# Performance work log

Hardware: AMD Instinct MI355X
Metric: run time of the kernel (lower is better)

The kernel has to match this reference:

```python
import jax, jax.numpy as jnp
from jax import lax
import numpy as np

MAXMAG = 10.0   # max_residue_magnitude
DG = 16         # deformable_groups
K = 9           # 3x3 kernel taps


def _conv(x, w, b):
    return lax.conv_general_dilated(x, w, (1, 1), 'SAME',
                                    dimension_numbers=('NCHW', 'OIHW', 'NCHW')) + b[None, :, None, None]


def _lrelu(v):
    return jnp.where(v >= 0, v, 0.1 * v)


def _sample(img, py, px):
    # img [C,H,W]; py,px [K,H,W] absolute sample coords; bilinear, zeros outside (torchvision semantics)
    H, W = img.shape[1], img.shape[2]
    y0 = jnp.floor(py)
    x0 = jnp.floor(px)
    wy1 = py - y0
    wx1 = px - x0

    def gather(yi, xi):
        valid = ((yi >= 0) & (yi < H) & (xi >= 0) & (xi < W)).astype(img.dtype)
        yc = jnp.clip(yi, 0, H - 1).astype(jnp.int32)
        xc = jnp.clip(xi, 0, W - 1).astype(jnp.int32)
        return img[:, yc, xc] * valid[None]  # [C,K,H,W]

    v00 = gather(y0, x0)
    v01 = gather(y0, x0 + 1)
    v10 = gather(y0 + 1, x0)
    v11 = gather(y0 + 1, x0 + 1)
    return (v00 * ((1 - wy1) * (1 - wx1))[None] + v01 * ((1 - wy1) * wx1)[None]
            + v10 * (wy1 * (1 - wx1))[None] + v11 * (wy1 * wx1)[None])


def setup_inputs() -> dict:
    key = jax.random.key(0)
    ks = jax.random.split(key, 12)
    N, CIN, COUT, H, W = 4, 128, 64, 96, 96
    f = lambda k, sh, s: jax.random.normal(k, sh, dtype=jnp.float32) * s
    return {
        'x': f(ks[0], (N, CIN, H, W), 1.0),
        'extra_feat': f(ks[1], (N, 3 * COUT, H, W), 1.0),
        'flow_1': f(ks[2], (N, 2, H, W), 2.0),
        'flow_2': f(ks[3], (N, 2, H, W), 2.0),
        'w_off0': f(ks[4], (COUT, 3 * COUT + 4, 3, 3), 0.02), 'b_off0': jnp.zeros((COUT,), jnp.float32),
        'w_off1': f(ks[5], (COUT, COUT, 3, 3), 0.04), 'b_off1': jnp.zeros((COUT,), jnp.float32),
        'w_off2': f(ks[6], (COUT, COUT, 3, 3), 0.04), 'b_off2': jnp.zeros((COUT,), jnp.float32),
        'w_off3': f(ks[7], (27 * DG, COUT, 3, 3), 0.02), 'b_off3': jnp.zeros((27 * DG,), jnp.float32),
        'w_dcn': f(ks[8], (COUT, CIN, 3, 3), 0.03), 'b_dcn': jnp.zeros((COUT,), jnp.float32),
    }


def reference(x, extra_feat, flow_1, flow_2, w_off0, b_off0, w_off1, b_off1,
              w_off2, b_off2, w_off3, b_off3, w_dcn, b_dcn):
    N, CIN, H, W = x.shape
    COUT = w_dcn.shape[0]
    Cg = CIN // DG
    # conv_offset stack on cat([extra_feat, flow_1, flow_2])
    feat = jnp.concatenate([extra_feat, flow_1, flow_2], axis=1)
    h = _lrelu(_conv(feat, w_off0, b_off0))
    h = _lrelu(_conv(h, w_off1, b_off1))
    h = _lrelu(_conv(h, w_off2, b_off2))
    out = _conv(h, w_off3, b_off3)                      # [N, 27*DG, H, W]
    o1, o2, mask = jnp.split(out, 3, axis=1)            # each [N, 9*DG, H, W]
    offs = MAXMAG * jnp.tanh(jnp.concatenate([o1, o2], axis=1))
    off1, off2 = jnp.split(offs, 2, axis=1)
    # flow.flip(1) -> (dy, dx); repeat interleaves over the 72 (tap) pairs
    off1 = off1 + jnp.tile(flow_1[:, ::-1], (1, off1.shape[1] // 2, 1, 1))
    off2 = off2 + jnp.tile(flow_2[:, ::-1], (1, off2.shape[1] // 2, 1, 1))
    # torchvision layout: channel c = g*2*K + 2*k + {y,x}; groups 0..7 <- off1, 8..15 <- off2
    off = jnp.concatenate([off1, off2], axis=1).reshape(N, DG, K, 2, H, W)
    m = jax.nn.sigmoid(mask).reshape(N, DG, K, H, W)
    # absolute sampling positions per tap
    kk = jnp.arange(K)
    ky = (kk // 3 - 1).astype(x.dtype)[:, None, None]
    kx = (kk % 3 - 1).astype(x.dtype)[:, None, None]
    gy = jnp.arange(H, dtype=x.dtype)[:, None]
    gx = jnp.arange(W, dtype=x.dtype)[None, :]
    py = off[:, :, :, 0] + ky + gy                      # [N,DG,K,H,W]
    px = off[:, :, :, 1] + kx + gx
    xg = x.reshape(N, DG, Cg, H, W)
    sampled = jax.vmap(jax.vmap(_sample))(xg, py, px)   # [N,DG,Cg,K,H,W]
    wg = w_dcn.reshape(COUT, DG, Cg, K)
    y = jnp.einsum('ngckhw,ogck->nohw', sampled * m[:, :, None], wg)
    return y + b_dcn[None, :, None, None]
```

## Files before the change

kernel.cpp:

```cpp
#include <hip/hip_runtime.h>
#include <math.h>

#define NB 4
#define HH 96
#define WW 96
#define HW (HH*WW)
#define NPIX (NB*HW)
#define C_IN 128
#define C_OUT 64
#define DGRP 16
#define CG 8

typedef short v8s __attribute__((ext_vector_type(8)));
typedef float v4f __attribute__((ext_vector_type(4)));
typedef unsigned short u16;
typedef unsigned int u32;

__device__ __forceinline__ u16 f2bf(float x) {
    u32 u = __float_as_uint(x);
    u32 r = (u + 0x7FFFu + ((u >> 16) & 1u)) >> 16;
    return (u16)r;
}
__device__ __forceinline__ float lo_bf(u32 w) { return __uint_as_float(w << 16); }
__device__ __forceinline__ float hi_bf(u32 w) { return __uint_as_float(w & 0xFFFF0000u); }
__device__ __forceinline__ float ftanh(float x) {
    float e = __expf(2.0f * x);
    return 1.0f - 2.0f / (e + 1.0f);
}
__device__ __forceinline__ float fsigm(float x) {
    return 1.0f / (1.0f + __expf(-x));
}
__device__ __forceinline__ v8s u4_to_v8s(uint4 q) {
    union { uint4 q; v8s s; } u; u.q = q; return u.s;
}
__device__ __forceinline__ u32 cvtpk(float a, float b) {
    u32 r;
    asm("v_cvt_pk_bf16_f32 %0, %1, %2" : "=v"(r) : "v"(a), "v"(b));
    return r;
}
__device__ __forceinline__ u16 f16of(float a) {
    u32 r;
    asm("v_cvt_f16_f32 %0, %1" : "=v"(r) : "v"(a));
    return (u16)r;
}
__device__ __forceinline__ float f16lo(u32 w) {
    float r;
    asm("v_cvt_f32_f16 %0, %1" : "=v"(r) : "v"(w));
    return r;
}
__device__ __forceinline__ float f16hi(u32 w) { return f16lo(w >> 16); }

__global__ __launch_bounds__(256) void prep_catT(
    const float* __restrict__ ef, const float* __restrict__ f1,
    const float* __restrict__ f2, u16* __restrict__ catT)
{
    __shared__ float T[64][65];
    const int t   = threadIdx.x;
    const int p   = blockIdx.x * 64;
    const int ch0 = blockIdx.y * 64;
    const int n   = p / HW;
    const int rem = p - n * HW;
    const int px  = t & 63;
    const int wv  = t >> 6;
    #pragma unroll
    for (int kk = 0; kk < 16; ++kk) {
        int chl = wv * 16 + kk;
        int ch  = ch0 + chl;
        float v = 0.f;
        if (ch < 192)      v = ef[(size_t)(n * 192 + ch) * HW + rem + px];
        else if (ch < 194) v = f1[(size_t)(n * 2 + (ch - 192)) * HW + rem + px];
        else if (ch < 196) v = f2[(size_t)(n * 2 + (ch - 194)) * HW + rem + px];
        T[chl][px] = v;
    }
    __syncthreads();
    const int s = t & 7;
    #pragma unroll
    for (int it = 0; it < 2; ++it) {
        int pxo = (t >> 3) + it * 32;
        u32 w0 = (u32)f2bf(T[s*8+0][pxo]) | ((u32)f2bf(T[s*8+1][pxo]) << 16);
        u32 w1 = (u32)f2bf(T[s*8+2][pxo]) | ((u32)f2bf(T[s*8+3][pxo]) << 16);
        u32 w2 = (u32)f2bf(T[s*8+4][pxo]) | ((u32)f2bf(T[s*8+5][pxo]) << 16);
        u32 w3 = (u32)f2bf(T[s*8+6][pxo]) | ((u32)f2bf(T[s*8+7][pxo]) << 16);
        *(uint4*)&catT[((size_t)(p + pxo)) * 256 + ch0 + s * 8] = make_uint4(w0, w1, w2, w3);
    }
}

__global__ __launch_bounds__(256) void prep_xT(
    const float* __restrict__ x, u16* __restrict__ xT)
{
    __shared__ float T[64][65];
    const int t   = threadIdx.x;
    const int p   = blockIdx.x * 64;
    const int ch0 = blockIdx.y * 64;
    const int n   = p / HW;
    const int rem = p - n * HW;
    const int px  = t & 63;
    const int wv  = t >> 6;
    #pragma unroll
    for (int kk = 0; kk < 16; ++kk) {
        int chl = wv * 16 + kk;
        T[chl][px] = x[(size_t)(n * C_IN + ch0 + chl) * HW + rem + px];
    }
    __syncthreads();
    const int s = t & 7;
    #pragma unroll
    for (int it = 0; it < 2; ++it) {
        int pxo = (t >> 3) + it * 32;
        u32 w0 = (u32)f2bf(T[s*8+0][pxo]) | ((u32)f2bf(T[s*8+1][pxo]) << 16);
        u32 w1 = (u32)f2bf(T[s*8+2][pxo]) | ((u32)f2bf(T[s*8+3][pxo]) << 16);
        u32 w2 = (u32)f2bf(T[s*8+4][pxo]) | ((u32)f2bf(T[s*8+5][pxo]) << 16);
        u32 w3 = (u32)f2bf(T[s*8+6][pxo]) | ((u32)f2bf(T[s*8+7][pxo]) << 16);
        *(uint4*)&xT[((size_t)(ch0 / 8 + s) * NPIX + (p + pxo)) * 8] = make_uint4(w0, w1, w2, w3);
    }
}

__device__ __forceinline__ void pack_wf_one(
    const float* __restrict__ w, u16* __restrict__ wp,
    int Cout, int CoutPad, int CIN, int CIP, int idx)
{
    const int NKF = CIP / 32, NOG = CoutPad / 16;
    int c    = idx & 7;
    int ln   = (idx >> 3) & 63;
    int rest = idx >> 9;
    int og   = rest % NOG; rest /= NOG;
    int kfg  = rest % NKF;
    int tap  = rest / NKF;
    int l15 = ln & 15, lg = ln >> 4;
    int o  = og * 16 + l15;
    int ci = kfg * 32 + lg * 8 + c;
    float v = (o < Cout && ci < CIN) ? w[((size_t)o * CIN + ci) * 9 + tap] : 0.f;
    wp[idx] = f2bf(v);
}

__global__ __launch_bounds__(256) void pack_all(
    const float* __restrict__ w0, u16* __restrict__ w0p,
    const float* __restrict__ w1, u16* __restrict__ w1p,
    const float* __restrict__ w2, u16* __restrict__ w2p,
    const float* __restrict__ w3, u16* __restrict__ w3p,
    const float* __restrict__ wd, u16* __restrict__ wdf)
{
    int idx = blockIdx.x * 256 + threadIdx.x;
    if (idx < 147456) { pack_wf_one(w0, w0p, 64, 64, 196, 256, idx); return; }
    idx -= 147456;
    if (idx < 36864)  { pack_wf_one(w1, w1p, 64, 64, 64, 64, idx); return; }
    idx -= 36864;
    if (idx < 36864)  { pack_wf_one(w2, w2p, 64, 64, 64, 64, idx); return; }
    idx -= 36864;
    if (idx < 258048) { pack_wf_one(w3, w3p, 432, 448, 64, 64, idx); return; }
    idx -= 258048;
    {
        int c  = idx & 7;
        int ln = (idx >> 3) & 63;
        int m  = (idx >> 9) & 3;
        int kk = idx >> 11;
        int l15 = ln & 15, lg = ln >> 4;
        int o = m * 16 + l15;
        int slot = kk * 4 + lg;
        int g = slot / 9, kt = slot - 9 * g;
        wdf[idx] = f2bf(wd[((size_t)(o * C_IN + g * CG + c)) * 9 + kt]);
    }
}

template<int CIP, int NCHUNK, int OST, bool LRELU, bool TOUT, int NOB>
__global__ __launch_bounds__(256) void conv_mfma(
    const u16* __restrict__ inT,
    const u16* __restrict__ wp,
    const float* __restrict__ bias,
    int CoutReal,
    u16* __restrict__ outT,
    u32* __restrict__ pairT,
    u16* __restrict__ maskT)
{
    constexpr int COLS  = (NOB > 1) ? 100 : 50;
    constexpr int LTILE = 3 * COLS * 64;
    constexpr int LSZ   = (NCHUNK > 1) ? 2 * LTILE : LTILE;
    constexpr int NKF   = CIP / 32;
    constexpr int NOG   = OST / 16;
    __shared__ __align__(16) u16 L[LSZ];

    const int t   = threadIdx.x;
    const int tb  = blockIdx.x;
    const int row = (NOB > 1) ? tb : (tb >> 1);
    const int p0  = (NOB > 1) ? 0 : (tb & 1) * 48;
    const int n   = row / HH;
    const int h   = row - n * HH;
    const int ln  = t & 63;
    const int wv  = t >> 6;
    const int l15 = ln & 15;
    const int lg  = ln >> 4;

    auto stage = [&](int ch, int buf) {
        const int cb = ch * 64;
        const int NCOL = (NOB > 1) ? 98 : 50;
        const int NTASK = 3 * NCOL * 8;
        u16* Lb = &L[buf * LTILE];
        #pragma unroll
        for (int it = 0; it < (NTASK + 255) / 256; ++it) {
            int task = it * 256 + t;
            if (task < NTASK) {
                int s  = task & 7;
                int cl = task >> 3;
                int r3 = cl / NCOL;
                int c  = cl - r3 * NCOL;
                int yy = h + r3 - 1;
                int xx = p0 + c - 1;
                uint4 v = make_uint4(0u, 0u, 0u, 0u);
                if ((unsigned)yy < HH && (unsigned)xx < WW)
                    v = *(const uint4*)&inT[((size_t)(n * HW + yy * WW + xx)) * CIP + cb + s * 8];
                *(uint4*)&Lb[(r3 * COLS + c) * 64 + ((s ^ (c & 7)) * 8)] = v;
            }
        }
    };

    if constexpr (NOB == 1) {
        v4f acc[3];
        #pragma unroll
        for (int i = 0; i < 3; ++i) acc[i] = (v4f){0.f, 0.f, 0.f, 0.f};

        stage(0, 0);
        for (int ch = 0; ch < NCHUNK; ++ch) {
            __syncthreads();
            if (ch + 1 < NCHUNK) stage(ch + 1, (ch + 1) & 1);
            const u16* Lb = &L[(ch & 1) * LTILE];
            #pragma unroll
            for (int tap = 0; tap < 9; ++tap) {
                const int ty = tap / 3, tx = tap - ty * 3;
                #pragma unroll
                for (int kf = 0; kf < 2; ++kf) {
                    v8s b = *(const v8s*)&wp[((((size_t)tap * NKF + (ch * 2 + kf)) * NOG + wv) * 64 + ln) * 8];
                    #pragma unroll
                    for (int fm = 0; fm < 3; ++fm) {
                        int c = fm * 16 + l15 + tx;
                        v8s a = *(const v8s*)&Lb[(ty * COLS + c) * 64 + (((kf * 4 + lg) ^ (c & 7)) * 8)];
                        acc[fm] = __builtin_amdgcn_mfma_f32_16x16x32_bf16(a, b, acc[fm], 0, 0, 0);
                    }
                }
            }
        }

        int o = wv * 16 + l15;
        float bv = (o < CoutReal) ? bias[o] : 0.f;
        #pragma unroll
        for (int fm = 0; fm < 3; ++fm) {
            #pragma unroll
            for (int r = 0; r < 4; ++r) {
                int px = p0 + fm * 16 + lg * 4 + r;
                float v = acc[fm][r] + bv;
                if (LRELU) v = (v >= 0.f) ? v : 0.1f * v;
                outT[((size_t)(n * HW + h * WW + px)) * OST + o] = f2bf(v);
            }
        }
    } else {
        stage(0, 0);
        __syncthreads();
        const size_t gpix = (size_t)n * HW + h * WW;
        const int ob_lo = blockIdx.y * 4;
        const int ob_hi = (ob_lo + 4 < NOB) ? ob_lo + 4 : NOB;

        for (int ob = ob_lo; ob < ob_hi; ++ob) {
            const int obase = ob * 64 + wv * 16;
            if (obase >= 432) continue;

            v4f acc[6];
            #pragma unroll
            for (int i = 0; i < 6; ++i) acc[i] = (v4f){0.f, 0.f, 0.f, 0.f};

            #pragma unroll
            for (int tap = 0; tap < 9; ++tap) {
                const int ty = tap / 3, tx = tap - ty * 3;
                #pragma unroll
                for (int kf = 0; kf < 2; ++kf) {
                    v8s bw = *(const v8s*)&wp[((((size_t)tap * NKF + kf) * NOG + (ob * 4 + wv)) * 64 + ln) * 8];
                    #pragma unroll
                    for (int fm = 0; fm < 6; ++fm) {
                        int c = fm * 16 + l15 + tx;
                        v8s a = *(const v8s*)&L[(ty * COLS + c) * 64 + (((kf * 4 + lg) ^ (c & 7)) * 8)];
                        acc[fm] = __builtin_amdgcn_mfma_f32_16x16x32_bf16(bw, a, acc[fm], 0, 0, 0);
                    }
                }
            }

            float bv[4];
            #pragma unroll
            for (int r = 0; r < 4; ++r) bv[r] = bias[obase + lg * 4 + r];

            if (obase < 288) {
                const int pr = (obase + lg * 4) >> 1;
                #pragma unroll
                for (int fm = 0; fm < 6; ++fm) {
                    const size_t pix = gpix + fm * 16 + l15;
                    float ty0 = 10.0f * ftanh(acc[fm][0] + bv[0]);
                    float tx0 = 10.0f * ftanh(acc[fm][1] + bv[1]);
                    float ty1 = 10.0f * ftanh(acc[fm][2] + bv[2]);
                    float tx1 = 10.0f * ftanh(acc[fm][3] + bv[3]);
                    u32 v0 = (u32)f16of(ty0) | ((u32)f16of(tx0) << 16);
                    u32 v1 = (u32)f16of(ty1) | ((u32)f16of(tx1) << 16);
                    pairT[(size_t)pr * NPIX + pix]       = v0;
                    pairT[(size_t)(pr + 1) * NPIX + pix] = v1;
                }
            } else {
                #pragma unroll
                for (int fm = 0; fm < 6; ++fm) {
                    const size_t pix = gpix + fm * 16 + l15;
                    #pragma unroll
                    for (int r = 0; r < 4; ++r) {
                        int mch = obase + lg * 4 + r - 288;
                        maskT[(size_t)mch * NPIX + pix] = f16of(fsigm(acc[fm][r] + bv[r]));
                    }
                }
            }
        }
    }
}

__global__ __launch_bounds__(256) void dcn_fused(
    const u16* __restrict__ xT,
    const float* __restrict__ f1,
    const float* __restrict__ f2,
    const u32*  __restrict__ pairT,
    const u16*  __restrict__ maskT,
    const u16*  __restrict__ wdf,
    const float* __restrict__ bdcn,
    float* __restrict__ part)
{
    const int t    = threadIdx.x;
    const int xb   = blockIdx.x;
    const int xw   = (xb & 7) * 72 + (xb >> 3);
    const int p0   = xw * 64;
    const int ks   = blockIdx.y;
    const int ln   = t & 63;
    const int wv   = t >> 6;
    const int l15  = ln & 15;
    const int lg   = ln >> 4;
    const int n    = p0 / HW;
    const int rem0 = p0 - n * HW;
    const int p    = p0 + wv * 16 + l15;
    const int rem  = rem0 + wv * 16 + l15;
    const int h    = rem / WW;
    const int w    = rem - h * WW;

    const char* pTc = (const char*)pairT;
    const char* mTc = (const char*)maskT;
    const char* xTc = (const char*)xT;
    const u32 p4   = (u32)p << 2;
    const u32 p2   = (u32)p << 1;
    const u32 nb16 = (u32)(n * HW) << 4;

    const float f1yh = f1[(size_t)(n * 2 + 1) * HW + rem] + (float)h;
    const float f1xw = f1[(size_t)(n * 2 + 0) * HW + rem] + (float)w;
    const float f2yh = f2[(size_t)(n * 2 + 1) * HW + rem] + (float)h;
    const float f2xw = f2[(size_t)(n * 2 + 0) * HW + rem] + (float)w;

    auto scal = [&](int sl, u32& yx, u32& mr) {
        yx = *(const u32*)(pTc + ((u32)sl * (u32)(NPIX * 4) + p4));
        mr = (u32)*(const u16*)(mTc + ((u32)sl * (u32)(NPIX * 2) + p2));
    };

    auto coords = [&](int sl, u32 yx, u32 mr,
                      uint4& q00, uint4& q01, uint4& q10, uint4& q11,
                      float& w00, float& w01, float& w10, float& w11) {
        const int g  = (sl * 57) >> 9;
        const int kt = sl - 9 * g;
        const int ky = (kt * 11) >> 5;
        const int kx = kt - 3 * ky;
        const float fy = (g < 8) ? f1yh : f2yh;
        const float fx = (g < 8) ? f1xw : f2xw;
        const float py  = f16lo(yx) + (fy + (float)(ky - 1));
        const float pxx = f16hi(yx) + (fx + (float)(kx - 1));
        const float m   = f16lo(mr);

        const float y0f = floorf(py), x0f = floorf(pxx);
        const int   iy0 = (int)y0f,   ix0 = (int)x0f;
        const float wy = py - y0f, wx = pxx - x0f;
        const bool v0y = ((unsigned)iy0 < HH);
        const bool v1y = ((unsigned)(iy0 + 1) < HH);
        const bool v0x = ((unsigned)ix0 < WW);
        const bool v1x = ((unsigned)(ix0 + 1) < WW);
        const float wy0m = (1.0f - wy) * m, wy1m = wy * m;
        w00 = (v0y && v0x) ? wy0m * (1.0f - wx) : 0.0f;
        w01 = (v0y && v1x) ? wy0m * wx          : 0.0f;
        w10 = (v1y && v0x) ? wy1m * (1.0f - wx) : 0.0f;
        w11 = (v1y && v1x) ? wy1m * wx          : 0.0f;

        const int iy0c = min(max(iy0, 0), HH - 1);
        const int iy1c = min(max(iy0 + 1, 0), HH - 1);
        const int ix0c = min(max(ix0, 0), WW - 1);
        const int ix1c = min(max(ix0 + 1, 0), WW - 1);
        const u32 gof = (u32)g * (u32)(NPIX * 16) + nb16;
        const u32 r0  = gof + (u32)iy0c * (u32)(WW * 16);
        const u32 r1  = gof + (u32)iy1c * (u32)(WW * 16);
        const u32 c0  = (u32)ix0c << 4;
        const u32 c1  = (u32)ix1c << 4;
        q00 = *(const uint4*)(xTc + (r0 + c0));
        q01 = *(const uint4*)(xTc + (r0 + c1));
        q10 = *(const uint4*)(xTc + (r1 + c0));
        q11 = *(const uint4*)(xTc + (r1 + c1));
    };

    auto blend = [&](const uint4& q00, const uint4& q01,
                     const uint4& q10, const uint4& q11,
                     float w00, float w01, float w10, float w11) -> v8s {
        u32 pv0 = cvtpk(
            w00*lo_bf(q00.x) + w01*lo_bf(q01.x) + w10*lo_bf(q10.x) + w11*lo_bf(q11.x),
            w00*hi_bf(q00.x) + w01*hi_bf(q01.x) + w10*hi_bf(q10.x) + w11*hi_bf(q11.x));
        u32 pv1 = cvtpk(
            w00*lo_bf(q00.y) + w01*lo_bf(q01.y) + w10*lo_bf(q10.y) + w11*lo_bf(q11.y),
            w00*hi_bf(q00.y) + w01*hi_bf(q01.y) + w10*hi_bf(q10.y) + w11*hi_bf(q11.y));
        u32 pv2 = cvtpk(
            w00*lo_bf(q00.z) + w01*lo_bf(q01.z) + w10*lo_bf(q10.z) + w11*lo_bf(q11.z),
            w00*hi_bf(q00.z) + w01*hi_bf(q01.z) + w10*hi_bf(q10.z) + w11*hi_bf(q11.z));
        u32 pv3 = cvtpk(
            w00*lo_bf(q00.w) + w01*lo_bf(q01.w) + w10*lo_bf(q10.w) + w11*lo_bf(q11.w),
            w00*hi_bf(q00.w) + w01*hi_bf(q01.w) + w10*hi_bf(q10.w) + w11*hi_bf(q11.w));
        return u4_to_v8s(make_uint4(pv0, pv1, pv2, pv3));
    };

    v4f acc[4];
    #pragma unroll
    for (int i = 0; i < 4; ++i) acc[i] = (v4f){0.f, 0.f, 0.f, 0.f};

    const int cc0 = ks * 12;
    const int sb  = cc0 * 4 + lg;
    const char* wb = (const char*)wdf + ((u32)cc0 << 12) + ((u32)ln << 4);

    uint4 qA00, qA01, qA10, qA11;  float wA00, wA01, wA10, wA11;
    uint4 qB00, qB01, qB10, qB11;  float wB00, wB01, wB10, wB11;
    u32 yxN, mrN;

    {
        u32 yx, mr;
        scal(sb, yx, mr);
        coords(sb, yx, mr, qA00, qA01, qA10, qA11, wA00, wA01, wA10, wA11);
        scal(sb + 4, yx, mr);
        coords(sb + 4, yx, mr, qB00, qB01, qB10, qB11, wB00, wB01, wB10, wB11);
        scal(sb + 8, yxN, mrN);
    }

    #pragma unroll 1
    for (int j = 0; j < 12; j += 2) {
        {
            const char* wj = wb + ((u32)j << 12);
            v8s aW0 = *(const v8s*)(wj);
            v8s aW1 = *(const v8s*)(wj + 1024);
            v8s aW2 = *(const v8s*)(wj + 2048);
            v8s aW3 = *(const v8s*)(wj + 3072);
            v8s bP = blend(qA00, qA01, qA10, qA11, wA00, wA01, wA10, wA11);
            acc[0] = __builtin_amdgcn_mfma_f32_16x16x32_bf16(bP, aW0, acc[0], 0, 0, 0);
            acc[1] = __builtin_amdgcn_mfma_f32_16x16x32_bf16(bP, aW1, acc[1], 0, 0, 0);
            acc[2] = __builtin_amdgcn_mfma_f32_16x16x32_bf16(bP, aW2, acc[2], 0, 0, 0);
            acc[3] = __builtin_amdgcn_mfma_f32_16x16x32_bf16(bP, aW3, acc[3], 0, 0, 0);
            if (j + 2 < 12)
                coords(sb + (j + 2) * 4, yxN, mrN,
                       qA00, qA01, qA10, qA11, wA00, wA01, wA10, wA11);
            if (j + 3 < 12) scal(sb + (j + 3) * 4, yxN, mrN);
        }
        {
            const char* wj = wb + ((u32)(j + 1) << 12);
            v8s aW0 = *(const v8s*)(wj);
            v8s aW1 = *(const v8s*)(wj + 1024);
            v8s aW2 = *(const v8s*)(wj + 2048);
            v8s aW3 = *(const v8s*)(wj + 3072);
            v8s bP = blend(qB00, qB01, qB10, qB11, wB00, wB01, wB10, wB11);
            acc[0] = __builtin_amdgcn_mfma_f32_16x16x32_bf16(bP, aW0, acc[0], 0, 0, 0);
            acc[1] = __builtin_amdgcn_mfma_f32_16x16x32_bf16(bP, aW1, acc[1], 0, 0, 0);
            acc[2] = __builtin_amdgcn_mfma_f32_16x16x32_bf16(bP, aW2, acc[2], 0, 0, 0);
            acc[3] = __builtin_amdgcn_mfma_f32_16x16x32_bf16(bP, aW3, acc[3], 0, 0, 0);
            if (j + 3 < 12)
                coords(sb + (j + 3) * 4, yxN, mrN,
                       qB00, qB01, qB10, qB11, wB00, wB01, wB10, wB11);
            if (j + 4 < 12) scal(sb + (j + 4) * 4, yxN, mrN);
        }
    }

    float* yp = part + (size_t)ks * ((size_t)NPIX * C_OUT);
    #pragma unroll
    for (int m = 0; m < 4; ++m) {
        const int o = m * 16 + l15;
        const float bd = (ks == 0) ? bdcn[o] : 0.0f;
        const size_t idx = (size_t)(n * C_OUT + o) * HW + rem0 + wv * 16 + lg * 4;
        *(float4*)&yp[idx] = make_float4(acc[m][0] + bd, acc[m][1] + bd,
                                         acc[m][2] + bd, acc[m][3] + bd);
    }
}

__global__ __launch_bounds__(256) void dcn_reduce(
    const float* __restrict__ part, float* __restrict__ y)
{
    const size_t i = ((size_t)blockIdx.x * 256 + threadIdx.x) * 4;
    const size_t S = (size_t)NPIX * C_OUT;
    float4 a = *(const float4*)&part[i];
    float4 b = *(const float4*)&part[i + S];
    float4 c = *(const float4*)&part[i + 2 * S];
    *(float4*)&y[i] = make_float4(a.x + b.x + c.x, a.y + b.y + c.y,
                                  a.z + b.z + c.z, a.w + b.w + c.w);
}

extern "C" void kernel_launch(void* const* d_in, const int* in_sizes, int n_in,
                              void* d_out, int out_size, void* d_ws, size_t ws_size,
                              hipStream_t stream) {
    const float* x  = (const float*)d_in[0];
    const float* ef = (const float*)d_in[1];
    const float* f1 = (const float*)d_in[2];
    const float* f2 = (const float*)d_in[3];
    const float* w0 = (const float*)d_in[4];
    const float* b0 = (const float*)d_in[5];
    const float* w1 = (const float*)d_in[6];
    const float* b1 = (const float*)d_in[7];
    const float* w2 = (const float*)d_in[8];
    const float* b2 = (const float*)d_in[9];
    const float* w3 = (const float*)d_in[10];
    const float* b3 = (const float*)d_in[11];
    const float* wd = (const float*)d_in[12];
    const float* bd = (const float*)d_in[13];
    float* y = (float*)d_out;
    char* wsb = (char*)d_ws;

    u16* catT  = (u16*)(wsb + 0);
    u16* h0T   = (u16*)(wsb + 18874368);
    u16* h1T   = (u16*)(wsb + 23592960);
    u16* h2T   = (u16*)(wsb + 28311552);
    u32* pairT = (u32*)(wsb + 33030144);
    u16* maskT = (u16*)(wsb + 54263808);
    u16* w0p   = (u16*)(wsb + 64880640);
    u16* w1p   = (u16*)(wsb + 65175552);
    u16* w2p   = (u16*)(wsb + 65249280);
    u16* w3p   = (u16*)(wsb + 65323008);
    u16* wdf   = (u16*)(wsb + 65839104);
    u16* xT    = (u16*)(wsb + 65986560);
    float* part = (float*)(wsb + 0);

    prep_catT<<<dim3(NPIX / 64, 4), 256, 0, stream>>>(ef, f1, f2, catT);
    prep_xT  <<<dim3(NPIX / 64, 2), 256, 0, stream>>>(x, xT);
    pack_all <<<dim3(552960 / 256), 256, 0, stream>>>(
        w0, w0p, w1, w1p, w2, w2p, w3, w3p, wd, wdf);

    conv_mfma<256, 4, 64, true,  false, 1><<<dim3(768), 256, 0, stream>>>(
        catT, w0p, b0, 64, h0T, nullptr, nullptr);
    conv_mfma< 64, 1, 64, true,  false, 1><<<dim3(768), 256, 0, stream>>>(
        h0T, w1p, b1, 64, h1T, nullptr, nullptr);
    conv_mfma< 64, 1, 64, true,  false, 1><<<dim3(768), 256, 0, stream>>>(
        h1T, w2p, b2, 64, h2T, nullptr, nullptr);
    conv_mfma< 64, 1, 448, false, true, 7><<<dim3(NB * HH, 2), 256, 0, stream>>>(
        h2T, w3p, b3, 432, nullptr, pairT, maskT);

    dcn_fused<<<dim3(NPIX / 64, 3), 256, 0, stream>>>(
        xT, f1, f2, pairT, maskT, wdf, bd, part);
    dcn_reduce<<<dim3(NPIX * C_OUT / 4 / 256), 256, 0, stream>>>(part, y);
}
```

Baseline: 134.5 us.

## Switch deformable sampling path from bf16 to packed fp16 blend and f16 MFMA

The transposed input and DCN weights are now stored as fp16 instead of bf16. The bilinear blend runs as packed half2 FMAs with pre-packed per-corner weights instead of unpacking to fp32 and repacking, and the MFMAs switch to the f16 variant. Offset and mask loads and the partial-output stores are also marked nontemporal. This cuts VALU work in the sampling inner loop, at the cost of fp16 accumulation inside the blend and fp16 range limits on the inputs.

```diff
diff --git a/kernel.cpp b/kernel.cpp
--- a/kernel.cpp
+++ b/kernel.cpp
@@ -13,6 +13,8 @@
 
 typedef short v8s __attribute__((ext_vector_type(8)));
 typedef float v4f __attribute__((ext_vector_type(4)));
+typedef _Float16 f16x2 __attribute__((ext_vector_type(2)));
+typedef _Float16 f16x8 __attribute__((ext_vector_type(8)));
 typedef unsigned short u16;
 typedef unsigned int u32;
 
@@ -21,8 +23,6 @@
     u32 r = (u + 0x7FFFu + ((u >> 16) & 1u)) >> 16;
     return (u16)r;
 }
-__device__ __forceinline__ float lo_bf(u32 w) { return __uint_as_float(w << 16); }
-__device__ __forceinline__ float hi_bf(u32 w) { return __uint_as_float(w & 0xFFFF0000u); }
 __device__ __forceinline__ float ftanh(float x) {
     float e = __expf(2.0f * x);
     return 1.0f - 2.0f / (e + 1.0f);
@@ -30,14 +30,14 @@
 __device__ __forceinline__ float fsigm(float x) {
     return 1.0f / (1.0f + __expf(-x));
 }
-__device__ __forceinline__ v8s u4_to_v8s(uint4 q) {
-    union { uint4 q; v8s s; } u; u.q = q; return u.s;
-}
-__device__ __forceinline__ u32 cvtpk(float a, float b) {
+__device__ __forceinline__ u32 pkrtz(float a, float b) {
     u32 r;
-    asm("v_cvt_pk_bf16_f32 %0, %1, %2" : "=v"(r) : "v"(a), "v"(b));
+    asm("v_cvt_pkrtz_f16_f32 %0, %1, %2" : "=v"(r) : "v"(a), "v"(b));
     return r;
 }
+__device__ __forceinline__ f16x2 u2h(u32 u) { union { u32 u; f16x2 h; } c; c.u = u; return c.h; }
+__device__ __forceinline__ u32 h2u(f16x2 h) { union { f16x2 h; u32 u; } c; c.h = h; return c.u; }
+__device__ __forceinline__ f16x8 q2h8(uint4 q) { union { uint4 q; f16x8 h; } c; c.q = q; return c.h; }
 __device__ __forceinline__ u16 f16of(float a) {
     u32 r;
     asm("v_cvt_f16_f32 %0, %1" : "=v"(r) : "v"(a));
@@ -106,10 +106,10 @@
     #pragma unroll
     for (int it = 0; it < 2; ++it) {
         int pxo = (t >> 3) + it * 32;
-        u32 w0 = (u32)f2bf(T[s*8+0][pxo]) | ((u32)f2bf(T[s*8+1][pxo]) << 16);
-        u32 w1 = (u32)f2bf(T[s*8+2][pxo]) | ((u32)f2bf(T[s*8+3][pxo]) << 16);
-        u32 w2 = (u32)f2bf(T[s*8+4][pxo]) | ((u32)f2bf(T[s*8+5][pxo]) << 16);
-        u32 w3 = (u32)f2bf(T[s*8+6][pxo]) | ((u32)f2bf(T[s*8+7][pxo]) << 16);
+        u32 w0 = pkrtz(T[s*8+0][pxo], T[s*8+1][pxo]);
+        u32 w1 = pkrtz(T[s*8+2][pxo], T[s*8+3][pxo]);
+        u32 w2 = pkrtz(T[s*8+4][pxo], T[s*8+5][pxo]);
+        u32 w3 = pkrtz(T[s*8+6][pxo], T[s*8+7][pxo]);
         *(uint4*)&xT[((size_t)(ch0 / 8 + s) * NPIX + (p + pxo)) * 8] = make_uint4(w0, w1, w2, w3);
     }
 }
@@ -157,7 +157,7 @@
         int o = m * 16 + l15;
         int slot = kk * 4 + lg;
         int g = slot / 9, kt = slot - 9 * g;
-        wdf[idx] = f2bf(wd[((size_t)(o * C_IN + g * CG + c)) * 9 + kt]);
+        wdf[idx] = f16of(wd[((size_t)(o * C_IN + g * CG + c)) * 9 + kt]);
     }
 }
 
@@ -289,12 +289,10 @@
                 #pragma unroll
                 for (int fm = 0; fm < 6; ++fm) {
                     const size_t pix = gpix + fm * 16 + l15;
-                    float ty0 = 10.0f * ftanh(acc[fm][0] + bv[0]);
-                    float tx0 = 10.0f * ftanh(acc[fm][1] + bv[1]);
-                    float ty1 = 10.0f * ftanh(acc[fm][2] + bv[2]);
-                    float tx1 = 10.0f * ftanh(acc[fm][3] + bv[3]);
-                    u32 v0 = (u32)f16of(ty0) | ((u32)f16of(tx0) << 16);
-                    u32 v1 = (u32)f16of(ty1) | ((u32)f16of(tx1) << 16);
+                    u32 v0 = pkrtz(10.0f * ftanh(acc[fm][0] + bv[0]),
+                                   10.0f * ftanh(acc[fm][1] + bv[1]));
+                    u32 v1 = pkrtz(10.0f * ftanh(acc[fm][2] + bv[2]),
+                                   10.0f * ftanh(acc[fm][3] + bv[3]));
                     pairT[(size_t)pr * NPIX + pix]       = v0;
                     pairT[(size_t)(pr + 1) * NPIX + pix] = v1;
                 }
@@ -352,13 +350,15 @@
     const float f2xw = f2[(size_t)(n * 2 + 0) * HW + rem] + (float)w;
 
     auto scal = [&](int sl, u32& yx, u32& mr) {
-        yx = *(const u32*)(pTc + ((u32)sl * (u32)(NPIX * 4) + p4));
-        mr = (u32)*(const u16*)(mTc + ((u32)sl * (u32)(NPIX * 2) + p2));
+        yx = __builtin_nontemporal_load(
+                 (const u32*)(pTc + ((u32)sl * (u32)(NPIX * 4) + p4)));
+        mr = (u32)__builtin_nontemporal_load(
+                 (const u16*)(mTc + ((u32)sl * (u32)(NPIX * 2) + p2)));
     };
 
     auto coords = [&](int sl, u32 yx, u32 mr,
                       uint4& q00, uint4& q01, uint4& q10, uint4& q11,
-                      float& w00, float& w01, float& w10, float& w11) {
+                      u32& W00, u32& W01, u32& W10, u32& W11) {
         const int g  = (sl * 57) >> 9;
         const int kt = sl - 9 * g;
         const int ky = (kt * 11) >> 5;
@@ -377,10 +377,12 @@
         const bool v0x = ((unsigned)ix0 < WW);
         const bool v1x = ((unsigned)(ix0 + 1) < WW);
         const float wy0m = (1.0f - wy) * m, wy1m = wy * m;
-        w00 = (v0y && v0x) ? wy0m * (1.0f - wx) : 0.0f;
-        w01 = (v0y && v1x) ? wy0m * wx          : 0.0f;
-        w10 = (v1y && v0x) ? wy1m * (1.0f - wx) : 0.0f;
-        w11 = (v1y && v1x) ? wy1m * wx          : 0.0f;
+        const float w00 = (v0y && v0x) ? wy0m * (1.0f - wx) : 0.0f;
+        const float w01 = (v0y && v1x) ? wy0m * wx          : 0.0f;
+        const float w10 = (v1y && v0x) ? wy1m * (1.0f - wx) : 0.0f;
+        const float w11 = (v1y && v1x) ? wy1m * wx          : 0.0f;
+        W00 = pkrtz(w00, w00);  W01 = pkrtz(w01, w01);
+        W10 = pkrtz(w10, w10);  W11 = pkrtz(w11, w11);
 
         const int iy0c = min(max(iy0, 0), HH - 1);
         const int iy1c = min(max(iy0 + 1, 0), HH - 1);
@@ -399,20 +401,19 @@
 
     auto blend = [&](const uint4& q00, const uint4& q01,
                      const uint4& q10, const uint4& q11,
-                     float w00, float w01, float w10, float w11) -> v8s {
-        u32 pv0 = cvtpk(
-            w00*lo_bf(q00.x) + w01*lo_bf(q01.x) + w10*lo_bf(q10.x) + w11*lo_bf(q11.x),
-            w00*hi_bf(q00.x) + w01*hi_bf(q01.x) + w10*hi_bf(q10.x) + w11*hi_bf(q11.x));
-        u32 pv1 = cvtpk(
-            w00*lo_bf(q00.y) + w01*lo_bf(q01.y) + w10*lo_bf(q10.y) + w11*lo_bf(q11.y),
-            w00*hi_bf(q00.y) + w01*hi_bf(q01.y) + w10*hi_bf(q10.y) + w11*hi_bf(q11.y));
-        u32 pv2 = cvtpk(
-            w00*lo_bf(q00.z) + w01*lo_bf(q01.z) + w10*lo_bf(q10.z) + w11*lo_bf(q11.z),
-            w00*hi_bf(q00.z) + w01*hi_bf(q01.z) + w10*hi_bf(q10.z) + w11*hi_bf(q11.z));
-        u32 pv3 = cvtpk(
-            w00*lo_bf(q00.w) + w01*lo_bf(q01.w) + w10*lo_bf(q10.w) + w11*lo_bf(q11.w),
-            w00*hi_bf(q00.w) + w01*hi_bf(q01.w) + w10*hi_bf(q10.w) + w11*hi_bf(q11.w));
-        return u4_to_v8s(make_uint4(pv0, pv1, pv2, pv3));
+                     u32 W00, u32 W01, u32 W10, u32 W11) -> uint4 {
+        const f16x2 A = u2h(W00), B = u2h(W01), C = u2h(W10), D = u2h(W11);
+        auto bl1 = [&](u32 a, u32 b, u32 c, u32 d) -> u32 {
+            f16x2 r = u2h(a) * A;
+            r = __builtin_elementwise_fma(u2h(b), B, r);
+            r = __builtin_elementwise_fma(u2h(c), C, r);
+            r = __builtin_elementwise_fma(u2h(d), D, r);
+            return h2u(r);
+        };
+        return make_uint4(bl1(q00.x, q01.x, q10.x, q11.x),
+                          bl1(q00.y, q01.y, q10.y, q11.y),
+                          bl1(q00.z, q01.z, q10.z, q11.z),
+                          bl1(q00.w, q01.w, q10.w, q11.w));
     };
 
     v4f acc[4];
@@ -423,16 +424,16 @@
     const int sb  = cc0 * 4 + lg;
     const char* wb = (const char*)wdf + ((u32)cc0 << 12) + ((u32)ln << 4);
 
-    uint4 qA00, qA01, qA10, qA11;  float wA00, wA01, wA10, wA11;
-    uint4 qB00, qB01, qB10, qB11;  float wB00, wB01, wB10, wB11;
+    uint4 qA00, qA01, qA10, qA11;  u32 WA00, WA01, WA10, WA11;
+    uint4 qB00, qB01, qB10, qB11;  u32 WB00, WB01, WB10, WB11;
     u32 yxN, mrN;
 
     {
         u32 yx, mr;
         scal(sb, yx, mr);
-        coords(sb, yx, mr, qA00, qA01, qA10, qA11, wA00, wA01, wA10, wA11);
+        coords(sb, yx, mr, qA00, qA01, qA10, qA11, WA00, WA01, WA10, WA11);
         scal(sb + 4, yx, mr);
-        coords(sb + 4, yx, mr, qB00, qB01, qB10, qB11, wB00, wB01, wB10, wB11);
+        coords(sb + 4, yx, mr, qB00, qB01, qB10, qB11, WB00, WB01, WB10, WB11);
         scal(sb + 8, yxN, mrN);
     }
 
@@ -440,34 +441,34 @@
     for (int j = 0; j < 12; j += 2) {
         {
             const char* wj = wb + ((u32)j << 12);
-            v8s aW0 = *(const v8s*)(wj);
-            v8s aW1 = *(const v8s*)(wj + 1024);
-            v8s aW2 = *(const v8s*)(wj + 2048);
-            v8s aW3 = *(const v8s*)(wj + 3072);
-            v8s bP = blend(qA00, qA01, qA10, qA11, wA00, wA01, wA10, wA11);
-            acc[0] = __builtin_amdgcn_mfma_f32_16x16x32_bf16(bP, aW0, acc[0], 0, 0, 0);
-            acc[1] = __builtin_amdgcn_mfma_f32_16x16x32_bf16(bP, aW1, acc[1], 0, 0, 0);
-            acc[2] = __builtin_amdgcn_mfma_f32_16x16x32_bf16(bP, aW2, acc[2], 0, 0, 0);
-            acc[3] = __builtin_amdgcn_mfma_f32_16x16x32_bf16(bP, aW3, acc[3], 0, 0, 0);
+            f16x8 aW0 = q2h8(*(const uint4*)(wj));
+            f16x8 aW1 = q2h8(*(const uint4*)(wj + 1024));
+            f16x8 aW2 = q2h8(*(const uint4*)(wj + 2048));
+            f16x8 aW3 = q2h8(*(const uint4*)(wj + 3072));
+            f16x8 bP = q2h8(blend(qA00, qA01, qA10, qA11, WA00, WA01, WA10, WA11));
+            acc[0] = __builtin_amdgcn_mfma_f32_16x16x32_f16(bP, aW0, acc[0], 0, 0, 0);
+            acc[1] = __builtin_amdgcn_mfma_f32_16x16x32_f16(bP, aW1, acc[1], 0, 0, 0);
+            acc[2] = __builtin_amdgcn_mfma_f32_16x16x32_f16(bP, aW2, acc[2], 0, 0, 0);
+            acc[3] = __builtin_amdgcn_mfma_f32_16x16x32_f16(bP, aW3, acc[3], 0, 0, 0);
             if (j + 2 < 12)
                 coords(sb + (j + 2) * 4, yxN, mrN,
-                       qA00, qA01, qA10, qA11, wA00, wA01, wA10, wA11);
+                       qA00, qA01, qA10, qA11, WA00, WA01, WA10, WA11);
             if (j + 3 < 12) scal(sb + (j + 3) * 4, yxN, mrN);
         }
         {
             const char* wj = wb + ((u32)(j + 1) << 12);
-            v8s aW0 = *(const v8s*)(wj);
-            v8s aW1 = *(const v8s*)(wj + 1024);
-            v8s aW2 = *(const v8s*)(wj + 2048);
-            v8s aW3 = *(const v8s*)(wj + 3072);
-            v8s bP = blend(qB00, qB01, qB10, qB11, wB00, wB01, wB10, wB11);
-            acc[0] = __builtin_amdgcn_mfma_f32_16x16x32_bf16(bP, aW0, acc[0], 0, 0, 0);
-            acc[1] = __builtin_amdgcn_mfma_f32_16x16x32_bf16(bP, aW1, acc[1], 0, 0, 0);
-            acc[2] = __builtin_amdgcn_mfma_f32_16x16x32_bf16(bP, aW2, acc[2], 0, 0, 0);
-            acc[3] = __builtin_amdgcn_mfma_f32_16x16x32_bf16(bP, aW3, acc[3], 0, 0, 0);
+            f16x8 aW0 = q2h8(*(const uint4*)(wj));
+            f16x8 aW1 = q2h8(*(const uint4*)(wj + 1024));
+            f16x8 aW2 = q2h8(*(const uint4*)(wj + 2048));
+            f16x8 aW3 = q2h8(*(const uint4*)(wj + 3072));
+            f16x8 bP = q2h8(blend(qB00, qB01, qB10, qB11, WB00, WB01, WB10, WB11));
+            acc[0] = __builtin_amdgcn_mfma_f32_16x16x32_f16(bP, aW0, acc[0], 0, 0, 0);
+            acc[1] = __builtin_amdgcn_mfma_f32_16x16x32_f16(bP, aW1, acc[1], 0, 0, 0);
+            acc[2] = __builtin_amdgcn_mfma_f32_16x16x32_f16(bP, aW2, acc[2], 0, 0, 0);
+            acc[3] = __builtin_amdgcn_mfma_f32_16x16x32_f16(bP, aW3, acc[3], 0, 0, 0);
             if (j + 3 < 12)
                 coords(sb + (j + 3) * 4, yxN, mrN,
-                       qB00, qB01, qB10, qB11, wB00, wB01, wB10, wB11);
+                       qB00, qB01, qB10, qB11, WB00, WB01, WB10, WB11);
             if (j + 4 < 12) scal(sb + (j + 4) * 4, yxN, mrN);
         }
     }
@@ -478,8 +479,8 @@
         const int o = m * 16 + l15;
         const float bd = (ks == 0) ? bdcn[o] : 0.0f;
         const size_t idx = (size_t)(n * C_OUT + o) * HW + rem0 + wv * 16 + lg * 4;
-        *(float4*)&yp[idx] = make_float4(acc[m][0] + bd, acc[m][1] + bd,
-                                         acc[m][2] + bd, acc[m][3] + bd);
+        v4f out = {acc[m][0] + bd, acc[m][1] + bd, acc[m][2] + bd, acc[m][3] + bd};
+        __builtin_nontemporal_store(out, (v4f*)&yp[idx]);
     }
 }
 
```

Result: slower. 147.5 us (+9.6%).
